# Optimization experiments

Measured on AMD Instinct MI355X. Metric: run time of the kernel, lower is better.

## Reference

```python
import jax, jax.numpy as jnp
import numpy as np

BLUR_KERNEL = [1, 3, 3, 1]
FACTOR = 2        # upsample factor U
KERNEL_SIZE = 3   # K of preceding transpose conv

# pad computation from Blur.__init__ (factor > 0 branch)
_P = len(BLUR_KERNEL) - FACTOR - (KERNEL_SIZE - 1)   # = 0
PAD0 = (_P + 1) // 2 + FACTOR - 1                    # = 1
PAD1 = _P // 2 + 1                                   # = 1


def make_kernel(k, factor):
    # stylegan2 make_kernel: normalized outer product, scaled by factor**2 for upsampling
    k = jnp.asarray(k, dtype=jnp.float32)
    k = k[None, :] * k[:, None]
    k = k / k.sum()
    return k * (factor ** 2)


def setup_inputs() -> dict:
    key = jax.random.key(0)
    # (N, C, (H-1)*U + K, (W-1)*U + K) with H=W=256, U=2, K=3 -> 513
    x = jax.random.normal(key, (4, 128, 513, 513), dtype=jnp.float32)
    kernel = make_kernel(BLUR_KERNEL, FACTOR)  # (4, 4) FIR buffer
    return {"input": x, "kernel": kernel}


def reference(input, kernel):
    # upfirdn2d with up=1, down=1, pad=(PAD0, PAD1): pad then true FIR convolution
    N, C, H, W = input.shape
    kh, kw = kernel.shape
    x = jnp.pad(input, ((0, 0), (0, 0), (PAD0, PAD1), (PAD0, PAD1)))
    # flip kernel: FIR convolution (torch native upfirdn2d flips before conv2d/cross-corr)
    w = jnp.flip(kernel, (0, 1)).astype(input.dtype)[None, None]  # (1,1,kh,kw)
    w = jnp.tile(w, (C, 1, 1, 1))                                  # depthwise (C,1,kh,kw)
    out = jax.lax.conv_general_dilated(
        x, w,
        window_strides=(1, 1),
        padding="VALID",
        dimension_numbers=("NCHW", "OIHW", "NCHW"),
        feature_group_count=C,
    )
    # out: (N, C, H + PAD0 + PAD1 - kh + 1, W + PAD0 + PAD1 - kw + 1) = (4,128,512,512)
    return out
```

## Files before the change

kernel.cpp:

```cpp
#include <hip/hip_runtime.h>


#define W_IN  513
#define H_IN  513
#define W_OUT 512
#define H_OUT 512
#define IN_PLANE  (W_IN * H_IN)
#define OUT_PLANE (W_OUT * H_OUT)

typedef float f4 __attribute__((ext_vector_type(4)));
typedef float f2 __attribute__((ext_vector_type(2)));

__device__ __forceinline__ f4 load4u(const float* p) {
    f4 v; __builtin_memcpy(&v, p, 16); return v;
}
__device__ __forceinline__ f2 load2u(const float* p) {
    f2 v; __builtin_memcpy(&v, p, 8); return v;
}

struct Win { f4 a, b; f2 c2; float m1; };

__global__ __launch_bounds__(256)
void blur_kernel(const float* __restrict__ in,
                 const float* __restrict__ kern,
                 float* __restrict__ out)
{
    const int t    = threadIdx.x;
    const int lane = t & 63;
    const int wv   = t >> 6;
    const int c    = lane << 3;
    const int cm1  = (c == 0) ? 0 : (c - 1);
    const int y0   = (blockIdx.x * 4 + wv) * 32;
    const int p    = blockIdx.y;

    const float* __restrict__ ip = in + (size_t)p * IN_PLANE;
    float* __restrict__ op = out + (size_t)p * OUT_PLANE + (size_t)y0 * W_OUT + c;

    const float kx0 = kern[2 * 4 + 3];
    const float kx1 = kern[2 * 4 + 2];
    const float kx2 = kern[2 * 4 + 1];
    const float kx3 = kern[2 * 4 + 0];
    const float inv = 1.0f / kx1;
    const float a0  = kern[3 * 4 + 2] * inv;
    const float a2  = kern[1 * 4 + 2] * inv;
    const float a3  = kern[0 * 4 + 2] * inv;

    const float mL = (c == 0)         ? 0.0f : 1.0f;
    const float mR = (c == W_OUT - 8) ? 0.0f : 1.0f;

    auto ldrow = [&](int ri, Win& w) {
        const int riC = ri < 0 ? 0 : (ri > H_IN - 1 ? H_IN - 1 : ri);
        const float* rp = ip + (size_t)riC * W_IN;
        w.m1 = rp[cm1];
        w.a  = load4u(rp + c);
        w.b  = load4u(rp + c + 4);
        w.c2 = load2u(rp + c + 8);
    };

    auto hcomp = [&](int ri, const Win& w, float* h) {
        const float rv = (ri >= 0 && ri < H_IN) ? 1.0f : 0.0f;
        const float k0 = kx0 * rv, k1 = kx1 * rv, k2 = kx2 * rv, k3 = kx3 * rv;
        float W[11];
        W[0]  = w.m1 * mL;
        W[1]  = w.a.x; W[2] = w.a.y; W[3] = w.a.z; W[4] = w.a.w;
        W[5]  = w.b.x; W[6] = w.b.y; W[7] = w.b.z; W[8] = w.b.w;
        W[9]  = w.c2.x;
        W[10] = w.c2.y * mR;
#pragma unroll
        for (int k = 0; k < 8; ++k)
            h[k] = W[k] * k0 + W[k + 1] * k1 + W[k + 2] * k2 + W[k + 3] * k3;
    };

    auto vstore = [&](int r, const float* h0, const float* h1,
                      const float* h2, const float* h3) {
        float o[8];
#pragma unroll
        for (int k = 0; k < 8; ++k)
            o[k] = a0 * h0[k] + h1[k] + a2 * h2[k] + a3 * h3[k];
        *reinterpret_cast<f4*>(op + (size_t)r * W_OUT)     = (f4){o[0], o[1], o[2], o[3]};
        *reinterpret_cast<f4*>(op + (size_t)r * W_OUT + 4) = (f4){o[4], o[5], o[6], o[7]};
    };

    Win L0, L1, L2, L3;
    float hA[8], hB[8], hC[8], hD[8];

    ldrow(y0 - 1, L0);
    ldrow(y0,     L1);
    ldrow(y0 + 1, L2);
    ldrow(y0 + 2, L3);
    hcomp(y0 - 1, L0, hA);
    hcomp(y0,     L1, hB);
    hcomp(y0 + 1, L2, hC);

    for (int r = 0; r < 32; r += 4) {
        ldrow(y0 + 3 + r, L0);
        hcomp(y0 + 2 + r, L3, hD);
        vstore(r,     hA, hB, hC, hD);

        ldrow(y0 + 4 + r, L1);
        hcomp(y0 + 3 + r, L0, hA);
        vstore(r + 1, hB, hC, hD, hA);

        ldrow(y0 + 5 + r, L2);
        hcomp(y0 + 4 + r, L1, hB);
        vstore(r + 2, hC, hD, hA, hB);

        ldrow(y0 + 6 + r, L3);
        hcomp(y0 + 5 + r, L2, hC);
        vstore(r + 3, hD, hA, hB, hC);
    }
}

extern "C" void kernel_launch(void* const* d_in, const int* in_sizes, int n_in,
                              void* d_out, int out_size, void* d_ws, size_t ws_size,
                              hipStream_t stream) {
    const float* x    = (const float*)d_in[0];
    const float* kern = (const float*)d_in[1];
    float* out        = (float*)d_out;

    dim3 grid(H_OUT / 128, 4 * 128, 1);
    dim3 block(256, 1, 1);
    blur_kernel<<<grid, block, 0, stream>>>(x, kern, out);
}
```

Baseline: 942.4 us.

## Deepen row prefetch ring to six buffers and use nontemporal output stores

Replaces the 4-deep row window rotation with a fully unrolled 6-entry ring, so each row is loaded three iterations before its horizontal pass uses it. This puts more loads in flight per wave to hide global memory latency. Output stores become nontemporal so the streamed results do not pollute cache. Full unrolling of 32 rows and extra window registers raise code size and register pressure, which could reduce occupancy.

```diff
diff --git a/kernel.cpp b/kernel.cpp
--- a/kernel.cpp
+++ b/kernel.cpp
@@ -77,37 +77,26 @@
 #pragma unroll
         for (int k = 0; k < 8; ++k)
             o[k] = a0 * h0[k] + h1[k] + a2 * h2[k] + a3 * h3[k];
-        *reinterpret_cast<f4*>(op + (size_t)r * W_OUT)     = (f4){o[0], o[1], o[2], o[3]};
-        *reinterpret_cast<f4*>(op + (size_t)r * W_OUT + 4) = (f4){o[4], o[5], o[6], o[7]};
+        f4 lo = (f4){o[0], o[1], o[2], o[3]};
+        f4 hi = (f4){o[4], o[5], o[6], o[7]};
+        __builtin_nontemporal_store(lo, reinterpret_cast<f4*>(op + (size_t)r * W_OUT));
+        __builtin_nontemporal_store(hi, reinterpret_cast<f4*>(op + (size_t)r * W_OUT + 4));
     };
 
-    Win L0, L1, L2, L3;
-    float hA[8], hB[8], hC[8], hD[8];
+    Win Wn[6];
+    float h[4][8];
 
-    ldrow(y0 - 1, L0);
-    ldrow(y0,     L1);
-    ldrow(y0 + 1, L2);
-    ldrow(y0 + 2, L3);
-    hcomp(y0 - 1, L0, hA);
-    hcomp(y0,     L1, hB);
-    hcomp(y0 + 1, L2, hC);
+#pragma unroll
+    for (int j = 0; j < 6; ++j) ldrow(y0 - 1 + j, Wn[j]);
+#pragma unroll
+    for (int j = 0; j < 3; ++j) hcomp(y0 - 1 + j, Wn[j], h[j]);
 
-    for (int r = 0; r < 32; r += 4) {
-        ldrow(y0 + 3 + r, L0);
-        hcomp(y0 + 2 + r, L3, hD);
-        vstore(r,     hA, hB, hC, hD);
-
-        ldrow(y0 + 4 + r, L1);
-        hcomp(y0 + 3 + r, L0, hA);
-        vstore(r + 1, hB, hC, hD, hA);
-
-        ldrow(y0 + 5 + r, L2);
-        hcomp(y0 + 4 + r, L1, hB);
-        vstore(r + 2, hC, hD, hA, hB);
-
-        ldrow(y0 + 6 + r, L3);
-        hcomp(y0 + 5 + r, L2, hC);
-        vstore(r + 3, hD, hA, hB, hC);
+#pragma unroll
+    for (int r = 0; r < 32; ++r) {
+        if (r <= 28)
+            ldrow(y0 + 5 + r, Wn[r % 6]);
+        hcomp(y0 + 2 + r, Wn[(r + 3) % 6], h[(r + 3) & 3]);
+        vstore(r, h[r & 3], h[(r + 1) & 3], h[(r + 2) & 3], h[(r + 3) & 3]);
     }
 }
 
```

Result: slower. 1.051 ms (+11.5%).
